# Kernel tuning notes

Hardware: AMD Instinct MI355X
Metric: run time of the kernel (lower is better)

The kernel has to match this reference:

```python
import jax, jax.numpy as jnp
import numpy as np
import math

EMBED_DIM = 1024
WINDOW = 512


def setup_inputs() -> dict:
    key = jax.random.key(0)
    k_x, k_mb, k_wg, k_bg = jax.random.split(key, 4)
    x = jax.random.normal(k_x, (4, 4096, EMBED_DIM), dtype=jnp.float32)
    memory_bank = jax.random.normal(k_mb, (WINDOW, EMBED_DIM), dtype=jnp.float32)
    # memory_gate: nn.Linear(embed_dim, embed_dim)
    lim = 1.0 / math.sqrt(EMBED_DIM)
    gate_w = jax.random.uniform(k_wg, (EMBED_DIM, EMBED_DIM), jnp.float32, -lim, lim)
    gate_b = jax.random.uniform(k_bg, (EMBED_DIM,), jnp.float32, -lim, lim)
    return {"x": x, "memory_bank": memory_bank, "gate_w": gate_w, "gate_b": gate_b}


def reference(x, memory_bank, gate_w, gate_b):
    d = x.shape[-1]
    # attention scores over fixed memory bank: [B, S, W]
    scores = jnp.einsum("bsd,wd->bsw", x, memory_bank) / jnp.sqrt(jnp.asarray(d, x.dtype))
    attn = jax.nn.softmax(scores, axis=-1)
    retrieved = jnp.einsum("bsw,wd->bsd", attn, memory_bank)
    gate = jax.nn.sigmoid(jnp.einsum("bsd,ed->bse", x, gate_w) + gate_b)
    return gate * x + (1.0 - gate) * retrieved
```

## Files before the change

kernel.cpp:

```cpp
#include <hip/hip_runtime.h>
#include <hip/hip_bf16.h>

#define EMBED 1024
#define WINDOW 512
#define NROWS 16384

typedef __attribute__((ext_vector_type(4))) float f32x4;
typedef __bf16 bf16x8 __attribute__((ext_vector_type(8)));

#define GLDS(g, l)                                                        \
  __builtin_amdgcn_global_load_lds(                                       \
      (const __attribute__((address_space(1))) void*)(const void*)(g),    \
      (__attribute__((address_space(3))) void*)(void*)(l), 16, 0, 0)

__global__ __launch_bounds__(256) void cast_bf16_kernel(
    const float* __restrict__ in, __bf16* __restrict__ out, int n8) {
  int i = blockIdx.x * blockDim.x + threadIdx.x;
  if (i >= n8) return;
  const f32x4* p = (const f32x4*)(in + (size_t)i * 8);
  f32x4 a = p[0], b = p[1];
  bf16x8 o = {(__bf16)a[0], (__bf16)a[1], (__bf16)a[2], (__bf16)a[3],
              (__bf16)b[0], (__bf16)b[1], (__bf16)b[2], (__bf16)b[3]};
  *(bf16x8*)(out + (size_t)i * 8) = o;
}

__global__ __launch_bounds__(256) void transpose_mb_kernel(
    const float* __restrict__ mb, __bf16* __restrict__ mbt) {
  int idx = blockIdx.x * blockDim.x + threadIdx.x;
  int w = idx >> 10, d = idx & 1023;
  mbt[(size_t)d * WINDOW + w] = (__bf16)mb[idx];
}

__global__ __launch_bounds__(512, 2) void scores_mega_kernel(
    const float* __restrict__ x, const __bf16* __restrict__ mbb,
    __bf16* __restrict__ xb, __bf16* __restrict__ s1) {
  __shared__ __align__(16) __bf16 ldsA[2][64 * 32];
  __shared__ __align__(16) __bf16 ldsB[2][512 * 32];
  __shared__ float sred[8][64];
  __shared__ float sfin[64];
  const int tid = threadIdx.x, lane = tid & 63, wave = tid >> 6;
  const int row0 = blockIdx.x * 64;
  const int warp_n = wave;
  const int fr = lane & 15, fq = lane >> 4;

  const int arow = tid >> 3;
  const int acol4 = (tid & 7) * 4;
  const int ag = (tid >> 1) & 3;
  const int ah = tid & 1;
  const int fA = (arow & 3) ^ ((arow >> 2) & 3);
  const int aws = arow * 32 + ((ag ^ fA) * 8) + ah * 4;
  const float* aSrc = x + (size_t)(row0 + arow) * EMBED + acol4;
  __bf16* xbDst = xb + (size_t)(row0 + arow) * EMBED + acol4;

  const int srow = lane >> 2;
  const int sgc = (lane & 3) ^ ((lane >> 2) & 3) ^ ((lane >> 4) & 3);
  const __bf16* bSrc = mbb + (size_t)(wave * 64 + srow) * EMBED + sgc * 8;

#define STG_B(t, buf)                                                         \
  {                                                                           \
    _Pragma("unroll") for (int c = 0; c < 4; ++c)                             \
        GLDS(bSrc + (size_t)c * 16 * EMBED + (t) * 32,                        \
             &ldsB[buf][(wave * 64 + c * 16) * 32]);                          \
  }

#define PACK_WRITE(av, buf, t)                                                \
  {                                                                           \
    unsigned u0 =                                                             \
        ((unsigned)__builtin_bit_cast(unsigned short, (__bf16)av[1]) << 16) | \
        (unsigned)__builtin_bit_cast(unsigned short, (__bf16)av[0]);          \
    unsigned u1 =                                                             \
        ((unsigned)__builtin_bit_cast(unsigned short, (__bf16)av[3]) << 16) | \
        (unsigned)__builtin_bit_cast(unsigned short, (__bf16)av[2]);          \
    uint2 w2 = {u0, u1};                                                      \
    *(uint2*)(&ldsA[buf][aws]) = w2;                                          \
    *(uint2*)(xbDst + (t) * 32) = w2;                                         \
  }

#define MCOMPUTE(cur)                                                         \
  {                                                                           \
    const __bf16* As_ = &ldsA[cur][0];                                        \
    const __bf16* Bs_ = &ldsB[cur][(warp_n * 64) * 32];                       \
    const int pg_ = (fq ^ ((fr & 3) ^ ((fr >> 2) & 3))) * 8;                  \
    bf16x8 af[4], bfv[4];                                                     \
    _Pragma("unroll") for (int m = 0; m < 4; ++m)                             \
        af[m] = *(const bf16x8*)(As_ + (m * 16 + fr) * 32 + pg_);             \
    _Pragma("unroll") for (int n = 0; n < 4; ++n)                             \
        bfv[n] = *(const bf16x8*)(Bs_ + (n * 16 + fr) * 32 + pg_);            \
    asm volatile("s_waitcnt lgkmcnt(0)" ::: "memory");                        \
    __builtin_amdgcn_s_setprio(1);                                            \
    _Pragma("unroll") for (int m = 0; m < 4; ++m)                             \
        _Pragma("unroll") for (int n = 0; n < 4; ++n)                         \
            acc[m][n] = __builtin_amdgcn_mfma_f32_16x16x32_bf16(              \
                af[m], bfv[n], acc[m][n], 0, 0, 0);                           \
    __builtin_amdgcn_s_setprio(0);                                            \
  }

  f32x4 acc[4][4];
#pragma unroll
  for (int m = 0; m < 4; ++m)
#pragma unroll
    for (int n = 0; n < 4; ++n) acc[m][n] = (f32x4){0.f, 0.f, 0.f, 0.f};

  {
    f32x4 a0 = *(const f32x4*)(aSrc);
    asm volatile("" ::: "memory");
    STG_B(0, 0);
    asm volatile("s_waitcnt vmcnt(0)" ::: "memory");
    PACK_WRITE(a0, 0, 0);
    asm volatile("s_waitcnt lgkmcnt(0)" ::: "memory");
    __builtin_amdgcn_s_barrier();
  }

  for (int t = 0; t < 32; ++t) {
    const int cur = t & 1;
    f32x4 an;
    if (t + 1 < 32) {
      an = *(const f32x4*)(aSrc + (t + 1) * 32);
      asm volatile("" ::: "memory");
      STG_B(t + 1, cur ^ 1);
    }
    MCOMPUTE(cur);
    if (t + 1 < 32) {
      asm volatile("s_waitcnt vmcnt(4)" ::: "memory");
      PACK_WRITE(an, cur ^ 1, t + 1);
      asm volatile("s_waitcnt vmcnt(1)" ::: "memory");
      asm volatile("s_waitcnt lgkmcnt(0)" ::: "memory");
    }
    __builtin_amdgcn_s_barrier();
  }
#undef STG_B
#undef PACK_WRITE
#undef MCOMPUTE

  const float scale = 0.03125f;
  float rmx[4][4];
#pragma unroll
  for (int m = 0; m < 4; ++m)
#pragma unroll
    for (int j = 0; j < 4; ++j) {
      float v = -1e30f;
#pragma unroll
      for (int n = 0; n < 4; ++n) {
        acc[m][n][j] *= scale;
        v = fmaxf(v, acc[m][n][j]);
      }
      rmx[m][j] = v;
    }
#pragma unroll
  for (int off = 1; off < 16; off <<= 1)
#pragma unroll
    for (int m = 0; m < 4; ++m)
#pragma unroll
      for (int j = 0; j < 4; ++j)
        rmx[m][j] = fmaxf(rmx[m][j], __shfl_xor(rmx[m][j], off));
  if (fr == 0) {
#pragma unroll
    for (int m = 0; m < 4; ++m)
#pragma unroll
      for (int j = 0; j < 4; ++j) sred[warp_n][m * 16 + fq * 4 + j] = rmx[m][j];
  }
  __syncthreads();
  if (tid < 64) {
    float v = sred[0][tid];
#pragma unroll
    for (int w = 1; w < 8; ++w) v = fmaxf(v, sred[w][tid]);
    sfin[tid] = v;
  }
  __syncthreads();

  float rsm[4][4];
#pragma unroll
  for (int m = 0; m < 4; ++m)
#pragma unroll
    for (int j = 0; j < 4; ++j) {
      const float fm = sfin[m * 16 + fq * 4 + j];
      float s = 0.f;
#pragma unroll
      for (int n = 0; n < 4; ++n) {
        float e = __expf(acc[m][n][j] - fm);
        acc[m][n][j] = e;
        s += e;
      }
      rsm[m][j] = s;
    }
#pragma unroll
  for (int off = 1; off < 16; off <<= 1)
#pragma unroll
    for (int m = 0; m < 4; ++m)
#pragma unroll
      for (int j = 0; j < 4; ++j) rsm[m][j] += __shfl_xor(rsm[m][j], off);
  if (fr == 0) {
#pragma unroll
    for (int m = 0; m < 4; ++m)
#pragma unroll
      for (int j = 0; j < 4; ++j) sred[warp_n][m * 16 + fq * 4 + j] = rsm[m][j];
  }
  __syncthreads();
  if (tid < 64) {
    float v = sred[0][tid];
#pragma unroll
    for (int w = 1; w < 8; ++w) v += sred[w][tid];
    sfin[tid] = 1.0f / v;
  }
  __syncthreads();

#pragma unroll
  for (int m = 0; m < 4; ++m)
#pragma unroll
    for (int j = 0; j < 4; ++j) {
      const int row = row0 + m * 16 + fq * 4 + j;
      const float inv = sfin[m * 16 + fq * 4 + j];
#pragma unroll
      for (int n = 0; n < 4; ++n)
        s1[(size_t)row * WINDOW + warp_n * 64 + n * 16 + fr] =
            (__bf16)(acc[m][n][j] * inv);
    }
}

__global__ __launch_bounds__(256, 2) void dual_fused128_kernel(
    const __bf16* __restrict__ s1, const __bf16* __restrict__ xb,
    const __bf16* __restrict__ mbt, const __bf16* __restrict__ gwb,
    const float* __restrict__ gb, float* __restrict__ out) {
  __shared__ __align__(16) __bf16 ldsA[2][128 * 64];
  __shared__ __align__(16) __bf16 ldsB[2][128 * 64];
  const int tid = threadIdx.x, lane = tid & 63, wave = tid >> 6;
  const int bid = blockIdx.x;
  const int xcd = bid & 7;
  const int g = bid >> 3;
  const int bm = xcd * 16 + (g >> 3);
  const int bn = g & 7;
  const int row0 = bm * 128, col0 = bn * 128;
  const int warp_m = wave >> 1, warp_n = wave & 1;
  const int fr = lane & 15, fq = lane >> 4;
  const int srow = lane >> 3;
  const int sgc = (lane & 7) ^ srow;
  const int wv32 = wave * 32;

  const __bf16* aR = s1 + (size_t)(row0 + wv32 + srow) * WINDOW + sgc * 8;
  const __bf16* bR = mbt + (size_t)(col0 + wv32 + srow) * WINDOW + sgc * 8;
  const __bf16* aG = xb + (size_t)(row0 + wv32 + srow) * EMBED + sgc * 8;
  const __bf16* bG = gwb + (size_t)(col0 + wv32 + srow) * EMBED + sgc * 8;

#define STG(vt, buf)                                                          \
  {                                                                           \
    if ((vt) < 8) {                                                           \
      const int k0_ = (vt)*64;                                                \
      _Pragma("unroll") for (int c = 0; c < 4; ++c)                           \
          GLDS(aR + (size_t)c * 8 * WINDOW + k0_,                             \
               &ldsA[buf][(wv32 + c * 8) * 64]);                              \
      _Pragma("unroll") for (int c = 0; c < 4; ++c)                           \
          GLDS(bR + (size_t)c * 8 * WINDOW + k0_,                             \
               &ldsB[buf][(wv32 + c * 8) * 64]);                              \
    } else {                                                                  \
      const int k0_ = ((vt)-8) * 64;                                          \
      _Pragma("unroll") for (int c = 0; c < 4; ++c)                           \
          GLDS(aG + (size_t)c * 8 * EMBED + k0_,                              \
               &ldsA[buf][(wv32 + c * 8) * 64]);                              \
      _Pragma("unroll") for (int c = 0; c < 4; ++c)                           \
          GLDS(bG + (size_t)c * 8 * EMBED + k0_,                              \
               &ldsB[buf][(wv32 + c * 8) * 64]);                              \
    }                                                                         \
  }

#define BARF                                                                  \
  {                                                                           \
    asm volatile("" ::: "memory");                                            \
    __builtin_amdgcn_s_barrier();                                             \
    asm volatile("" ::: "memory");                                            \
  }

#define COMPUTE(ACC, cur)                                                     \
  {                                                                           \
    const __bf16* As_ = &ldsA[cur][(warp_m * 64 + fr) * 64];                  \
    const __bf16* Bs_ = &ldsB[cur][(warp_n * 64 + fr) * 64];                  \
    _Pragma("unroll") for (int kk = 0; kk < 2; ++kk) {                        \
      const int pg_ = ((kk * 4 + fq) ^ (fr & 7)) * 8;                         \
      bf16x8 af[4], bfv[4];                                                   \
      _Pragma("unroll") for (int m = 0; m < 4; ++m)                           \
          af[m] = *(const bf16x8*)(As_ + m * 16 * 64 + pg_);                  \
      _Pragma("unroll") for (int n = 0; n < 4; ++n)                           \
          bfv[n] = *(const bf16x8*)(Bs_ + n * 16 * 64 + pg_);                 \
      __builtin_amdgcn_s_setprio(1);                                          \
      _Pragma("unroll") for (int m = 0; m < 4; ++m)                           \
          _Pragma("unroll") for (int n = 0; n < 4; ++n)                       \
              ACC[m][n] = __builtin_amdgcn_mfma_f32_16x16x32_bf16(            \
                  af[m], bfv[n], ACC[m][n], 0, 0, 0);                         \
      __builtin_amdgcn_s_setprio(0);                                          \
    }                                                                         \
  }

  f32x4 accr[4][4], accg[4][4];
#pragma unroll
  for (int m = 0; m < 4; ++m)
#pragma unroll
    for (int n = 0; n < 4; ++n) {
      accr[m][n] = (f32x4){0.f, 0.f, 0.f, 0.f};
      accg[m][n] = (f32x4){0.f, 0.f, 0.f, 0.f};
    }

  STG(0, 0);
  for (int vt = 0; vt < 8; ++vt) {
    const int cur = vt & 1;
    STG(vt + 1, cur ^ 1);
    asm volatile("s_waitcnt vmcnt(8)" ::: "memory");
    BARF;
    COMPUTE(accr, cur);
    BARF;
  }
  for (int vt = 8; vt < 24; ++vt) {
    const int cur = vt & 1;
    if (vt + 1 < 24) {
      STG(vt + 1, cur ^ 1);
      asm volatile("s_waitcnt vmcnt(8)" ::: "memory");
    } else {
      asm volatile("s_waitcnt vmcnt(0)" ::: "memory");
    }
    BARF;
    COMPUTE(accg, cur);
    BARF;
  }
#undef STG
#undef COMPUTE
#undef BARF

#pragma unroll
  for (int n = 0; n < 4; ++n) {
    const int col = col0 + warp_n * 64 + n * 16 + fr;
    const float bias = gb[col];
#pragma unroll
    for (int m = 0; m < 4; ++m) {
#pragma unroll
      for (int j = 0; j < 4; ++j) {
        const int row = row0 + warp_m * 64 + m * 16 + fq * 4 + j;
        const size_t o = (size_t)row * EMBED + col;
        const float gt = 1.0f / (1.0f + __expf(-(accg[m][n][j] + bias)));
        const float xv = (float)xb[o];
        out[o] = gt * xv + (1.0f - gt) * accr[m][n][j];
      }
    }
  }
}

extern "C" void kernel_launch(void* const* d_in, const int* in_sizes, int n_in,
                              void* d_out, int out_size, void* d_ws,
                              size_t ws_size, hipStream_t stream) {
  const float* x = (const float*)d_in[0];
  const float* mb = (const float*)d_in[1];
  const float* gw = (const float*)d_in[2];
  const float* gb = (const float*)d_in[3];
  float* out = (float*)d_out;

  char* ws = (char*)d_ws;
  __bf16* xb = (__bf16*)(ws);
  __bf16* mbb = (__bf16*)(ws + 33554432);
  __bf16* mbt = (__bf16*)(ws + 34603008);
  __bf16* gwb = (__bf16*)(ws + 35651584);
  __bf16* s1 = (__bf16*)(ws + 37748736);

  cast_bf16_kernel<<<256, 256, 0, stream>>>(mb, mbb, 65536);
  cast_bf16_kernel<<<512, 256, 0, stream>>>(gw, gwb, 131072);
  transpose_mb_kernel<<<2048, 256, 0, stream>>>(mb, mbt);
  scores_mega_kernel<<<256, 512, 0, stream>>>(x, mbb, xb, s1);
  dual_fused128_kernel<<<1024, 256, 0, stream>>>(s1, xb, mbt, gwb, gb, out);
}
```

Baseline: 123.6 us.

## Triple-buffer scores kernel pipeline and use LDS-tiled memory bank transpose

The scores kernel's K-loop moves from double to triple buffering. Loads for step t+2 are issued while step t computes, with adjusted vmcnt waits and rotating buffer indices. This raises LDS use and drops the launch bound to one block per CU. The memory-bank transpose now goes through a 32x33 shared-memory tile with vectorized reads and writes instead of strided scalar stores.

```diff
diff --git a/kernel.cpp b/kernel.cpp
--- a/kernel.cpp
+++ b/kernel.cpp
@@ -24,18 +24,31 @@
   *(bf16x8*)(out + (size_t)i * 8) = o;
 }
 
-__global__ __launch_bounds__(256) void transpose_mb_kernel(
+__global__ __launch_bounds__(256) void transpose_mb_lds_kernel(
     const float* __restrict__ mb, __bf16* __restrict__ mbt) {
-  int idx = blockIdx.x * blockDim.x + threadIdx.x;
-  int w = idx >> 10, d = idx & 1023;
-  mbt[(size_t)d * WINDOW + w] = (__bf16)mb[idx];
-}
-
-__global__ __launch_bounds__(512, 2) void scores_mega_kernel(
+  __shared__ __bf16 tile[32][33];
+  const int tx = threadIdx.x & 7, ty = threadIdx.x >> 3;
+  const int w0 = (blockIdx.x & 15) * 32;
+  const int d0 = (blockIdx.x >> 4) * 32;
+  f32x4 v = *(const f32x4*)(mb + (size_t)(w0 + ty) * EMBED + d0 + tx * 4);
+#pragma unroll
+  for (int j = 0; j < 4; ++j) tile[tx * 4 + j][ty] = (__bf16)v[j];
+  __syncthreads();
+  unsigned u0 =
+      ((unsigned)__builtin_bit_cast(unsigned short, tile[ty][tx * 4 + 1]) << 16) |
+      (unsigned)__builtin_bit_cast(unsigned short, tile[ty][tx * 4 + 0]);
+  unsigned u1 =
+      ((unsigned)__builtin_bit_cast(unsigned short, tile[ty][tx * 4 + 3]) << 16) |
+      (unsigned)__builtin_bit_cast(unsigned short, tile[ty][tx * 4 + 2]);
+  uint2 w2 = {u0, u1};
+  *(uint2*)(mbt + (size_t)(d0 + ty) * WINDOW + w0 + tx * 4) = w2;
+}
+
+__global__ __launch_bounds__(512, 1) void scores_mega_kernel(
     const float* __restrict__ x, const __bf16* __restrict__ mbb,
     __bf16* __restrict__ xb, __bf16* __restrict__ s1) {
-  __shared__ __align__(16) __bf16 ldsA[2][64 * 32];
-  __shared__ __align__(16) __bf16 ldsB[2][512 * 32];
+  __shared__ __align__(16) __bf16 ldsA[3][64 * 32];
+  __shared__ __align__(16) __bf16 ldsB[3][512 * 32];
   __shared__ float sred[8][64];
   __shared__ float sfin[64];
   const int tid = threadIdx.x, lane = tid & 63, wave = tid >> 6;
@@ -44,13 +57,12 @@
   const int fr = lane & 15, fq = lane >> 4;
 
   const int arow = tid >> 3;
-  const int acol4 = (tid & 7) * 4;
   const int ag = (tid >> 1) & 3;
   const int ah = tid & 1;
   const int fA = (arow & 3) ^ ((arow >> 2) & 3);
   const int aws = arow * 32 + ((ag ^ fA) * 8) + ah * 4;
-  const float* aSrc = x + (size_t)(row0 + arow) * EMBED + acol4;
-  __bf16* xbDst = xb + (size_t)(row0 + arow) * EMBED + acol4;
+  const float* aSrc = x + (size_t)(row0 + arow) * EMBED + (tid & 7) * 4;
+  __bf16* xbDst = xb + (size_t)(row0 + arow) * EMBED + (tid & 7) * 4;
 
   const int srow = lane >> 2;
   const int sgc = (lane & 3) ^ ((lane >> 2) & 3) ^ ((lane >> 4) & 3);
@@ -95,39 +107,58 @@
     __builtin_amdgcn_s_setprio(0);                                            \
   }
 
+#define TBODY(t, APACK, ALOAD)                                                \
+  {                                                                           \
+    if ((t) + 2 < 32) {                                                       \
+      ALOAD = *(const f32x4*)(aSrc + ((t) + 2) * 32);                         \
+      asm volatile("" ::: "memory");                                          \
+      STG_B((t) + 2, rs2);                                                    \
+    }                                                                         \
+    MCOMPUTE(rs0);                                                            \
+    if ((t) + 1 < 32) {                                                       \
+      if ((t) + 2 < 32) {                                                     \
+        asm volatile("s_waitcnt vmcnt(10)" ::: "memory");                     \
+      } else {                                                                \
+        asm volatile("s_waitcnt vmcnt(5)" ::: "memory");                      \
+      }                                                                       \
+      PACK_WRITE(APACK, rs1, (t) + 1);                                        \
+      if ((t) + 2 < 32) {                                                     \
+        asm volatile("s_waitcnt vmcnt(7)" ::: "memory");                      \
+      } else {                                                                \
+        asm volatile("s_waitcnt vmcnt(2)" ::: "memory");                      \
+      }                                                                       \
+      asm volatile("s_waitcnt lgkmcnt(0)" ::: "memory");                      \
+    }                                                                         \
+    __builtin_amdgcn_s_barrier();                                             \
+    const int tmp_ = rs0; rs0 = rs1; rs1 = rs2; rs2 = tmp_;                   \
+  }
+
   f32x4 acc[4][4];
 #pragma unroll
   for (int m = 0; m < 4; ++m)
 #pragma unroll
     for (int n = 0; n < 4; ++n) acc[m][n] = (f32x4){0.f, 0.f, 0.f, 0.f};
 
+  int rs0 = 0, rs1 = 1, rs2 = 2;
+  f32x4 aE, aO;
   {
     f32x4 a0 = *(const f32x4*)(aSrc);
     asm volatile("" ::: "memory");
     STG_B(0, 0);
-    asm volatile("s_waitcnt vmcnt(0)" ::: "memory");
+    aO = *(const f32x4*)(aSrc + 32);
+    asm volatile("" ::: "memory");
+    STG_B(1, 1);
+    asm volatile("s_waitcnt vmcnt(9)" ::: "memory");
     PACK_WRITE(a0, 0, 0);
     asm volatile("s_waitcnt lgkmcnt(0)" ::: "memory");
     __builtin_amdgcn_s_barrier();
   }
 
-  for (int t = 0; t < 32; ++t) {
-    const int cur = t & 1;
-    f32x4 an;
-    if (t + 1 < 32) {
-      an = *(const f32x4*)(aSrc + (t + 1) * 32);
-      asm volatile("" ::: "memory");
-      STG_B(t + 1, cur ^ 1);
-    }
-    MCOMPUTE(cur);
-    if (t + 1 < 32) {
-      asm volatile("s_waitcnt vmcnt(4)" ::: "memory");
-      PACK_WRITE(an, cur ^ 1, t + 1);
-      asm volatile("s_waitcnt vmcnt(1)" ::: "memory");
-      asm volatile("s_waitcnt lgkmcnt(0)" ::: "memory");
-    }
-    __builtin_amdgcn_s_barrier();
-  }
+  for (int t = 0; t < 32; t += 2) {
+    TBODY(t, aO, aE);
+    TBODY(t + 1, aE, aO);
+  }
+#undef TBODY
 #undef STG_B
 #undef PACK_WRITE
 #undef MCOMPUTE
@@ -359,7 +390,7 @@
 
   cast_bf16_kernel<<<256, 256, 0, stream>>>(mb, mbb, 65536);
   cast_bf16_kernel<<<512, 256, 0, stream>>>(gw, gwb, 131072);
-  transpose_mb_kernel<<<2048, 256, 0, stream>>>(mb, mbt);
+  transpose_mb_lds_kernel<<<512, 256, 0, stream>>>(mb, mbt);
   scores_mega_kernel<<<256, 512, 0, stream>>>(x, mbb, xb, s1);
   dual_fused128_kernel<<<1024, 256, 0, stream>>>(s1, xb, mbt, gwb, gb, out);
 }
```

Measured after the change: 122.9 us. About the same (-0.5%).
